# Performance work log

Hardware: AMD Instinct MI355X
Metric: run time of the kernel (lower is better)

The kernel has to match this reference:

```python
import jax, jax.numpy as jnp
import numpy as np

OUT_FEATURES = 11008
IN_FEATURES = 4096
GROUP_SIZE = 32
NUM_GROUPS = OUT_FEATURES * IN_FEATURES // GROUP_SIZE        # 1,409,024
NUM_PACKED = NUM_GROUPS * (GROUP_SIZE // 8 * 3)              # 16,908,288 bytes


def block_dequantize_3bit(weight_q3, weight_norm):
    """Unpack 3-bit codes (8 values per 3 bytes) and dequantize to fp32."""
    p = weight_q3.reshape(-1, 3).astype(jnp.int32)  # [N/8, 3] bytes
    b0, b1, b2 = p[:, 0], p[:, 1], p[:, 2]
    q = jnp.stack([
        b0 & 7,
        (b0 >> 3) & 7,
        ((b0 >> 6) & 3) | ((b1 & 1) << 2),
        (b1 >> 1) & 7,
        (b1 >> 4) & 7,
        ((b1 >> 7) & 1) | ((b2 & 3) << 1),
        (b2 >> 2) & 7,
        (b2 >> 5) & 7,
    ], axis=-1)                                     # [N/8, 8] codes in 0..7
    q = q.reshape(NUM_GROUPS, GROUP_SIZE).astype(jnp.float32)
    norm = weight_norm.astype(jnp.float32)[:, None]  # [num_groups, 1]
    w = (q / 7.0) * 2.0 * norm - norm                # map [0,7] -> [-norm, norm]
    return w.reshape(OUT_FEATURES, IN_FEATURES)


def setup_inputs() -> dict:
    key = jax.random.key(0)
    k1, k2, k3, k4 = jax.random.split(key, 4)
    x = jax.random.normal(k1, (4, 128, IN_FEATURES), dtype=jnp.float32)
    weight_q3 = jax.random.randint(k2, (NUM_PACKED,), 0, 256, dtype=jnp.int32)
    weight_norm = (jax.random.uniform(k3, (NUM_GROUPS,), dtype=jnp.float32) * 0.1 + 0.01).astype(jnp.float16)
    bias = jax.random.normal(k4, (OUT_FEATURES,), dtype=jnp.float32) * 0.02
    return {"x": x, "weight_q3": weight_q3, "weight_norm": weight_norm, "bias": bias}


def reference(x, weight_q3, weight_norm, bias):
    w = block_dequantize_3bit(weight_q3, weight_norm)  # [out, in] fp32
    return jnp.einsum('bsd,od->bso', x, w) + bias
```

## Files before the change

### kernel.cpp

```cpp
#include <hip/hip_runtime.h>
#include <hip/hip_fp16.h>

#define M_TOTAL 512
#define N_TOTAL 11008
#define K_TOTAL 4096
#define BM 64
#define BN 64
#define BK 64
#define NT (K_TOTAL / BK)
#define LDK 72

typedef short bf16x8 __attribute__((ext_vector_type(8)));
typedef float f32x4 __attribute__((ext_vector_type(4)));

__device__ __forceinline__ unsigned int pack2_bf16(float f0, float f1) {
    unsigned int u0 = __builtin_bit_cast(unsigned int, f0) + 0x8000u;
    unsigned int u1 = __builtin_bit_cast(unsigned int, f1) + 0x8000u;
    return (u0 >> 16) | (u1 & 0xFFFF0000u);
}

__device__ __forceinline__ void async_ld16(void* lds, const void* g) {
    __builtin_amdgcn_global_load_lds(
        (const __attribute__((address_space(1))) unsigned int*)g,
        (__attribute__((address_space(3))) unsigned int*)lds, 16, 0, 0);
}

__global__ void detect_norm_dtype(const void* __restrict__ wn, int* __restrict__ mode_out) {
    const int i = threadIdx.x;
    const unsigned short* u16 = (const unsigned short*)wn;
    const float* f32p = (const float*)wn;
    const float vb = __builtin_bit_cast(float, (unsigned int)u16[i] << 16);
    const float vh = __half2float(__builtin_bit_cast(__half, u16[i]));
    const float vf = f32p[i];
    const unsigned long long mb = __ballot(vb > 0.005f && vb < 0.12f);
    const unsigned long long mh = __ballot(vh > 0.005f && vh < 0.12f);
    const unsigned long long mf = __ballot(vf > 0.005f && vf < 0.12f);
    if (i == 0)
        *mode_out = (mb == ~0ull) ? 2 : ((mh == ~0ull) ? 1 : 0);
    (void)mf;
}

__global__ void __launch_bounds__(256)
convert_x_kernel(const float* __restrict__ x, unsigned short* __restrict__ xb) {
    const int i = (blockIdx.x * 256 + threadIdx.x) * 4;
    const float4 v = *(const float4*)&x[i];
    *(uint2*)&xb[i] = make_uint2(pack2_bf16(v.x, v.y), pack2_bf16(v.z, v.w));
}

__global__ void __launch_bounds__(256, 5)
l3b_gemm_pipe(const unsigned short* __restrict__ xb, const int* __restrict__ wq,
              const void* __restrict__ wnorm, const float* __restrict__ bias,
              float* __restrict__ out, const int* __restrict__ mode_ptr)
{
    __shared__ unsigned short As[2][BM * 64];
    __shared__ unsigned short Bs[2][BN * 64];

    const int mode = *mode_ptr;
    const int tid  = threadIdx.x;

    const int bid = blockIdx.x;
    const int w   = (bid & 7) * 172 + (bid >> 3);
    const int m0  = (w & 7) * BM;
    const int n0  = (w >> 3) * BN;

    const int wid  = tid >> 6;
    const int lane = tid & 63;
    const int quad = lane >> 4;
    const int lm   = lane & 15;
    const int wm   = (wid >> 1) * 32;
    const int wn   = (wid & 1) * 32;

    const int arow0 = wid * 8 + (lane >> 3);
    const int acol  = ((lane & 7) ^ ((lane >> 3) & 7)) * 8;
    const int aslot = (lane & 7) * 8;

    const int gin      = tid >> 1;
    const int half     = tid & 1;
    const int bn_local = gin >> 1;
    const int bkg      = gin & 1;
    const int c0       = bkg * 4 + half * 2;
    const int swz      = bn_local & 7;

    auto stageA = [&](int it, int buf) {
#pragma unroll
        for (int j = 0; j < 2; ++j) {
            const int row = arow0 + j * 32;
            async_ld16(&As[buf][(row << 6) + aslot],
                       &xb[(size_t)(m0 + row) * K_TOTAL + it * 64 + acol]);
        }
    };

    int2 w0a, w1a, w2a; float na;
    int2 w0b, w1b, w2b; float nb;

    auto loadNorm = [&](int g) -> float {
        if (mode == 0)      return ((const float*)wnorm)[g];
        else if (mode == 1) return __half2float(((const __half*)wnorm)[g]);
        else                return __builtin_bit_cast(float,
                               (unsigned int)((const unsigned short*)wnorm)[g] << 16);
    };
    auto loadB = [&](int it, int2& w0, int2& w1, int2& w2, float& nrm) {
        const int g    = (n0 + bn_local) * (K_TOTAL / 32) + it * 2 + bkg;
        const int base = g * 12 + half * 6;
        w0 = *(const int2*)&wq[base];
        w1 = *(const int2*)&wq[base + 2];
        w2 = *(const int2*)&wq[base + 4];
        nrm = loadNorm(g);
    };
    auto decodeB = [&](int2 w0, int2 w1, int2 w2, float nrm, int buf) {
        const float a = nrm * (2.0f / 7.0f);
        const float b = -nrm;
        const unsigned int bits0 =
            (unsigned)w0.x | ((unsigned)w0.y << 8) | ((unsigned)w1.x << 16);
        const unsigned int bits1 =
            (unsigned)w1.y | ((unsigned)w2.x << 8) | ((unsigned)w2.y << 16);
        unsigned int packs[8];
#pragma unroll
        for (int t3 = 0; t3 < 2; ++t3) {
            const unsigned int bits = t3 ? bits1 : bits0;
#pragma unroll
            for (int j = 0; j < 4; ++j) {
                const float f0 = fmaf((float)((bits >> (6 * j)) & 7), a, b);
                const float f1 = fmaf((float)((bits >> (6 * j + 3)) & 7), a, b);
                packs[t3 * 4 + j] = pack2_bf16(f0, f1);
            }
        }
        *(uint4*)&Bs[buf][(bn_local << 6) + ((c0 ^ swz) << 3)] =
            make_uint4(packs[0], packs[1], packs[2], packs[3]);
        *(uint4*)&Bs[buf][(bn_local << 6) + (((c0 + 1) ^ swz) << 3)] =
            make_uint4(packs[4], packs[5], packs[6], packs[7]);
    };

    f32x4 acc[2][2];
#pragma unroll
    for (int i = 0; i < 2; ++i)
#pragma unroll
        for (int j = 0; j < 2; ++j) acc[i][j] = (f32x4){0.f, 0.f, 0.f, 0.f};

    auto mfmaTile = [&](const unsigned short* Asb, const unsigned short* Bsb) {
#pragma unroll
        for (int ks = 0; ks < 2; ++ks) {
            const int cswz = (((ks * 4 + quad) ^ (lm & 7)) << 3);
            bf16x8 aF[2], bF[2];
#pragma unroll
            for (int mi = 0; mi < 2; ++mi)
                aF[mi] = *(const bf16x8*)&Asb[((wm + mi * 16 + lm) << 6) + cswz];
#pragma unroll
            for (int ni = 0; ni < 2; ++ni)
                bF[ni] = *(const bf16x8*)&Bsb[((wn + ni * 16 + lm) << 6) + cswz];
#pragma unroll
            for (int mi = 0; mi < 2; ++mi)
#pragma unroll
                for (int ni = 0; ni < 2; ++ni)
                    acc[mi][ni] = __builtin_amdgcn_mfma_f32_16x16x32_bf16(
                        aF[mi], bF[ni], acc[mi][ni], 0, 0, 0);
        }
    };

    stageA(0, 0);
    loadB(0, w0a, w1a, w2a, na);
    decodeB(w0a, w1a, w2a, na, 0);
    loadB(1, w0b, w1b, w2b, nb);
    __syncthreads();

    for (int it = 0; it < NT; it += 2) {
        if (it + 1 < NT) stageA(it + 1, 1);
        if (it + 2 < NT) loadB(it + 2, w0a, w1a, w2a, na);
        if (it + 1 < NT) decodeB(w0b, w1b, w2b, nb, 1);
        mfmaTile(As[0], Bs[0]);
        __syncthreads();

        if (it + 2 < NT) stageA(it + 2, 0);
        if (it + 3 < NT) loadB(it + 3, w0b, w1b, w2b, nb);
        if (it + 2 < NT) decodeB(w0a, w1a, w2a, na, 0);
        mfmaTile(As[1], Bs[1]);
        __syncthreads();
    }

#pragma unroll
    for (int ni = 0; ni < 2; ++ni) {
        const int o  = n0 + wn + ni * 16 + lm;
        const float bv = bias[o];
#pragma unroll
        for (int mi = 0; mi < 2; ++mi) {
#pragma unroll
            for (int r = 0; r < 4; ++r) {
                const int m = m0 + wm + mi * 16 + quad * 4 + r;
                out[m * N_TOTAL + o] = acc[mi][ni][r] + bv;
            }
        }
    }
}

__global__ void __launch_bounds__(256)
l3b_gemm_kernel(const float* __restrict__ x, const int* __restrict__ wq,
                const void* __restrict__ wnorm, const float* __restrict__ bias,
                float* __restrict__ out, const int* __restrict__ mode_ptr)
{
    __shared__ unsigned short As[128 * LDK];
    __shared__ unsigned short Bs[64 * LDK];

    const int mode = *mode_ptr;
    const int tid  = threadIdx.x;
    const int m0   = blockIdx.y * 128;
    const int n0   = blockIdx.x * 64;
    const int wid  = tid >> 6;
    const int lane = tid & 63;
    const int quad = lane >> 4;
    const int lm   = lane & 15;
    const int wm   = (wid >> 1) * 64;
    const int wn   = (wid & 1) * 32;

    f32x4 acc[4][2];
#pragma unroll
    for (int i = 0; i < 4; ++i)
#pragma unroll
        for (int j = 0; j < 2; ++j) acc[i][j] = (f32x4){0.f, 0.f, 0.f, 0.f};

    const int ar = tid >> 4;
    const int ac = (tid & 15) * 4;
    const int gin      = tid >> 1;
    const int half     = tid & 1;
    const int bn_local = gin >> 1;
    const int bkg      = gin & 1;

    for (int it = 0; it < NT; ++it) {
        const int k0 = it * BK;
        __syncthreads();
#pragma unroll
        for (int p = 0; p < 8; ++p) {
            const int row = p * 16 + ar;
            const float4 v = *(const float4*)&x[(m0 + row) * K_TOTAL + k0 + ac];
            *(uint2*)&As[row * LDK + ac] =
                make_uint2(pack2_bf16(v.x, v.y), pack2_bf16(v.z, v.w));
        }
        {
            const int g    = (n0 + bn_local) * (K_TOTAL / 32) + it * 2 + bkg;
            const int base = g * 12 + half * 6;
            const int2 w0 = *(const int2*)&wq[base];
            const int2 w1 = *(const int2*)&wq[base + 2];
            const int2 w2 = *(const int2*)&wq[base + 4];
            float nrm;
            if (mode == 0)      nrm = ((const float*)wnorm)[g];
            else if (mode == 1) nrm = __half2float(((const __half*)wnorm)[g]);
            else                nrm = __builtin_bit_cast(float,
                                    (unsigned int)((const unsigned short*)wnorm)[g] << 16);
            const float a = nrm * (2.0f / 7.0f);
            const float b = -nrm;
            const unsigned int bits0 =
                (unsigned)w0.x | ((unsigned)w0.y << 8) | ((unsigned)w1.x << 16);
            const unsigned int bits1 =
                (unsigned)w1.y | ((unsigned)w2.x << 8) | ((unsigned)w2.y << 16);
            unsigned int packs[8];
#pragma unroll
            for (int t3 = 0; t3 < 2; ++t3) {
                const unsigned int bits = t3 ? bits1 : bits0;
#pragma unroll
                for (int j = 0; j < 4; ++j) {
                    const float f0 = fmaf((float)((bits >> (6 * j)) & 7), a, b);
                    const float f1 = fmaf((float)((bits >> (6 * j + 3)) & 7), a, b);
                    packs[t3 * 4 + j] = pack2_bf16(f0, f1);
                }
            }
            unsigned int* dst = (unsigned int*)&Bs[bn_local * LDK + bkg * 32 + half * 16];
            *(uint4*)dst       = make_uint4(packs[0], packs[1], packs[2], packs[3]);
            *(uint4*)(dst + 4) = make_uint4(packs[4], packs[5], packs[6], packs[7]);
        }
        __syncthreads();
#pragma unroll
        for (int ks = 0; ks < 2; ++ks) {
            const int kb = ks * 32 + quad * 8;
            bf16x8 aF[4], bF[2];
#pragma unroll
            for (int mi = 0; mi < 4; ++mi)
                aF[mi] = *(const bf16x8*)&As[(wm + mi * 16 + lm) * LDK + kb];
#pragma unroll
            for (int ni = 0; ni < 2; ++ni)
                bF[ni] = *(const bf16x8*)&Bs[(wn + ni * 16 + lm) * LDK + kb];
#pragma unroll
            for (int mi = 0; mi < 4; ++mi)
#pragma unroll
                for (int ni = 0; ni < 2; ++ni)
                    acc[mi][ni] = __builtin_amdgcn_mfma_f32_16x16x32_bf16(
                        aF[mi], bF[ni], acc[mi][ni], 0, 0, 0);
        }
    }
#pragma unroll
    for (int ni = 0; ni < 2; ++ni) {
        const int o  = n0 + wn + ni * 16 + lm;
        const float bv = bias[o];
#pragma unroll
        for (int mi = 0; mi < 4; ++mi)
#pragma unroll
            for (int r = 0; r < 4; ++r) {
                const int m = m0 + wm + mi * 16 + quad * 4 + r;
                out[m * N_TOTAL + o] = acc[mi][ni][r] + bv;
            }
    }
}

extern "C" void kernel_launch(void* const* d_in, const int* in_sizes, int n_in,
                              void* d_out, int out_size, void* d_ws, size_t ws_size,
                              hipStream_t stream) {
    const float* x    = (const float*)d_in[0];
    const int*   wq   = (const int*)d_in[1];
    const void*  wn   = d_in[2];
    const float* bias = (const float*)d_in[3];
    float* out = (float*)d_out;
    int* mode = (int*)d_ws;

    detect_norm_dtype<<<1, 64, 0, stream>>>(wn, mode);

    const size_t need = 256 + (size_t)M_TOTAL * K_TOTAL * 2;
    if (ws_size >= need) {
        unsigned short* xb = (unsigned short*)((char*)d_ws + 256);
        convert_x_kernel<<<(M_TOTAL * K_TOTAL / 4) / 256, 256, 0, stream>>>(x, xb);
        l3b_gemm_pipe<<<(M_TOTAL / BM) * (N_TOTAL / BN), 256, 0, stream>>>(
            xb, wq, wn, bias, out, mode);
    } else {
        dim3 grid(N_TOTAL / 64, M_TOTAL / 128);
        l3b_gemm_kernel<<<grid, 256, 0, stream>>>(x, wq, wn, bias, out, mode);
    }
}
```

Measured before the change: 242.9 us.

## Use 128x64 tiles with 512 threads and fold dtype detection into GEMM

Doubles the M tile to 128 and the block to 512 threads, so each block covers twice the rows and each decoded weight tile is reused across more activations. B decode is split four ways per group, with each thread handling 8 codes instead of 16. The separate dtype-detection launch is replaced by each wave detecting the mode inline, which removes one kernel launch and a dependent global read. The trade-off is more LDS and registers per block and a grid that is half as large.

```diff
diff --git a/kernel.cpp b/kernel.cpp
--- a/kernel.cpp
+++ b/kernel.cpp
@@ -4,7 +4,7 @@
 #define M_TOTAL 512
 #define N_TOTAL 11008
 #define K_TOTAL 4096
-#define BM 64
+#define BM 128
 #define BN 64
 #define BK 64
 #define NT (K_TOTAL / BK)
@@ -25,19 +25,17 @@
         (__attribute__((address_space(3))) unsigned int*)lds, 16, 0, 0);
 }
 
-__global__ void detect_norm_dtype(const void* __restrict__ wn, int* __restrict__ mode_out) {
-    const int i = threadIdx.x;
+__device__ __forceinline__ int detect_mode_wave(const void* __restrict__ wn) {
+    const int lane = threadIdx.x & 63;
     const unsigned short* u16 = (const unsigned short*)wn;
     const float* f32p = (const float*)wn;
-    const float vb = __builtin_bit_cast(float, (unsigned int)u16[i] << 16);
-    const float vh = __half2float(__builtin_bit_cast(__half, u16[i]));
-    const float vf = f32p[i];
+    const float vb = __builtin_bit_cast(float, (unsigned int)u16[lane] << 16);
+    const float vh = __half2float(__builtin_bit_cast(__half, u16[lane]));
+    const float vf = f32p[lane];
     const unsigned long long mb = __ballot(vb > 0.005f && vb < 0.12f);
     const unsigned long long mh = __ballot(vh > 0.005f && vh < 0.12f);
-    const unsigned long long mf = __ballot(vf > 0.005f && vf < 0.12f);
-    if (i == 0)
-        *mode_out = (mb == ~0ull) ? 2 : ((mh == ~0ull) ? 1 : 0);
-    (void)mf;
+    (void)vf;
+    return (mb == ~0ull) ? 2 : ((mh == ~0ull) ? 1 : 0);
 }
 
 __global__ void __launch_bounds__(256)
@@ -47,51 +45,47 @@
     *(uint2*)&xb[i] = make_uint2(pack2_bf16(v.x, v.y), pack2_bf16(v.z, v.w));
 }
 
-__global__ void __launch_bounds__(256, 5)
+__global__ void __launch_bounds__(512, 6)
 l3b_gemm_pipe(const unsigned short* __restrict__ xb, const int* __restrict__ wq,
               const void* __restrict__ wnorm, const float* __restrict__ bias,
-              float* __restrict__ out, const int* __restrict__ mode_ptr)
+              float* __restrict__ out)
 {
     __shared__ unsigned short As[2][BM * 64];
     __shared__ unsigned short Bs[2][BN * 64];
 
-    const int mode = *mode_ptr;
     const int tid  = threadIdx.x;
+    const int mode = detect_mode_wave(wnorm);
 
     const int bid = blockIdx.x;
-    const int w   = (bid & 7) * 172 + (bid >> 3);
-    const int m0  = (w & 7) * BM;
-    const int n0  = (w >> 3) * BN;
+    const int w   = (bid & 7) * 86 + (bid >> 3);
+    const int m0  = (w & 3) * BM;
+    const int n0  = (w >> 2) * BN;
 
     const int wid  = tid >> 6;
     const int lane = tid & 63;
     const int quad = lane >> 4;
     const int lm   = lane & 15;
     const int wm   = (wid >> 1) * 32;
-    const int wn   = (wid & 1) * 32;
+    const int wn_  = (wid & 1) * 32;
 
     const int arow0 = wid * 8 + (lane >> 3);
     const int acol  = ((lane & 7) ^ ((lane >> 3) & 7)) * 8;
     const int aslot = (lane & 7) * 8;
 
-    const int gin      = tid >> 1;
-    const int half     = tid & 1;
-    const int bn_local = gin >> 1;
-    const int bkg      = gin & 1;
-    const int c0       = bkg * 4 + half * 2;
-    const int swz      = bn_local & 7;
+    const int gl   = tid >> 2;
+    const int sub  = tid & 3;
+    const int bn_l = gl >> 1;
+    const int kg   = gl & 1;
+    const int ldsB = (bn_l << 6) + ((((kg * 4 + sub)) ^ (bn_l & 7)) << 3);
 
     auto stageA = [&](int it, int buf) {
 #pragma unroll
         for (int j = 0; j < 2; ++j) {
-            const int row = arow0 + j * 32;
+            const int row = arow0 + j * 64;
             async_ld16(&As[buf][(row << 6) + aslot],
                        &xb[(size_t)(m0 + row) * K_TOTAL + it * 64 + acol]);
         }
     };
-
-    int2 w0a, w1a, w2a; float na;
-    int2 w0b, w1b, w2b; float nb;
 
     auto loadNorm = [&](int g) -> float {
         if (mode == 0)      return ((const float*)wnorm)[g];
@@ -99,36 +93,25 @@
         else                return __builtin_bit_cast(float,
                                (unsigned int)((const unsigned short*)wnorm)[g] << 16);
     };
-    auto loadB = [&](int it, int2& w0, int2& w1, int2& w2, float& nrm) {
-        const int g    = (n0 + bn_local) * (K_TOTAL / 32) + it * 2 + bkg;
-        const int base = g * 12 + half * 6;
-        w0 = *(const int2*)&wq[base];
-        w1 = *(const int2*)&wq[base + 2];
-        w2 = *(const int2*)&wq[base + 4];
+    auto loadB = [&](int it, int& b0, int& b1, int& b2, float& nrm) {
+        const int g    = (n0 + bn_l) * (K_TOTAL / 32) + it * 2 + kg;
+        const int base = g * 12 + sub * 3;
+        b0 = wq[base]; b1 = wq[base + 1]; b2 = wq[base + 2];
         nrm = loadNorm(g);
     };
-    auto decodeB = [&](int2 w0, int2 w1, int2 w2, float nrm, int buf) {
+    auto decodeB = [&](int b0, int b1, int b2, float nrm, int buf) {
         const float a = nrm * (2.0f / 7.0f);
         const float b = -nrm;
-        const unsigned int bits0 =
-            (unsigned)w0.x | ((unsigned)w0.y << 8) | ((unsigned)w1.x << 16);
-        const unsigned int bits1 =
-            (unsigned)w1.y | ((unsigned)w2.x << 8) | ((unsigned)w2.y << 16);
-        unsigned int packs[8];
-#pragma unroll
-        for (int t3 = 0; t3 < 2; ++t3) {
-            const unsigned int bits = t3 ? bits1 : bits0;
-#pragma unroll
-            for (int j = 0; j < 4; ++j) {
-                const float f0 = fmaf((float)((bits >> (6 * j)) & 7), a, b);
-                const float f1 = fmaf((float)((bits >> (6 * j + 3)) & 7), a, b);
-                packs[t3 * 4 + j] = pack2_bf16(f0, f1);
-            }
-        }
-        *(uint4*)&Bs[buf][(bn_local << 6) + ((c0 ^ swz) << 3)] =
-            make_uint4(packs[0], packs[1], packs[2], packs[3]);
-        *(uint4*)&Bs[buf][(bn_local << 6) + (((c0 + 1) ^ swz) << 3)] =
-            make_uint4(packs[4], packs[5], packs[6], packs[7]);
+        const unsigned int bits =
+            (unsigned)b0 | ((unsigned)b1 << 8) | ((unsigned)b2 << 16);
+        unsigned int packs[4];
+#pragma unroll
+        for (int j = 0; j < 4; ++j) {
+            const float f0 = fmaf((float)((bits >> (6 * j)) & 7), a, b);
+            const float f1 = fmaf((float)((bits >> (6 * j + 3)) & 7), a, b);
+            packs[j] = pack2_bf16(f0, f1);
+        }
+        *(uint4*)&Bs[buf][ldsB] = make_uint4(packs[0], packs[1], packs[2], packs[3]);
     };
 
     f32x4 acc[2][2];
@@ -147,7 +130,7 @@
                 aF[mi] = *(const bf16x8*)&Asb[((wm + mi * 16 + lm) << 6) + cswz];
 #pragma unroll
             for (int ni = 0; ni < 2; ++ni)
-                bF[ni] = *(const bf16x8*)&Bsb[((wn + ni * 16 + lm) << 6) + cswz];
+                bF[ni] = *(const bf16x8*)&Bsb[((wn_ + ni * 16 + lm) << 6) + cswz];
 #pragma unroll
             for (int mi = 0; mi < 2; ++mi)
 #pragma unroll
@@ -157,29 +140,32 @@
         }
     };
 
+    int b0a, b1a, b2a; float na;
+    int b0b, b1b, b2b; float nb;
+
     stageA(0, 0);
-    loadB(0, w0a, w1a, w2a, na);
-    decodeB(w0a, w1a, w2a, na, 0);
-    loadB(1, w0b, w1b, w2b, nb);
+    loadB(0, b0a, b1a, b2a, na);
+    decodeB(b0a, b1a, b2a, na, 0);
+    loadB(1, b0b, b1b, b2b, nb);
     __syncthreads();
 
     for (int it = 0; it < NT; it += 2) {
         if (it + 1 < NT) stageA(it + 1, 1);
-        if (it + 2 < NT) loadB(it + 2, w0a, w1a, w2a, na);
-        if (it + 1 < NT) decodeB(w0b, w1b, w2b, nb, 1);
+        if (it + 2 < NT) loadB(it + 2, b0a, b1a, b2a, na);
+        if (it + 1 < NT) decodeB(b0b, b1b, b2b, nb, 1);
         mfmaTile(As[0], Bs[0]);
         __syncthreads();
 
         if (it + 2 < NT) stageA(it + 2, 0);
-        if (it + 3 < NT) loadB(it + 3, w0b, w1b, w2b, nb);
-        if (it + 2 < NT) decodeB(w0a, w1a, w2a, na, 0);
+        if (it + 3 < NT) loadB(it + 3, b0b, b1b, b2b, nb);
+        if (it + 2 < NT) decodeB(b0a, b1a, b2a, na, 0);
         mfmaTile(As[1], Bs[1]);
         __syncthreads();
     }
 
 #pragma unroll
     for (int ni = 0; ni < 2; ++ni) {
-        const int o  = n0 + wn + ni * 16 + lm;
+        const int o  = n0 + wn_ + ni * 16 + lm;
         const float bv = bias[o];
 #pragma unroll
         for (int mi = 0; mi < 2; ++mi) {
@@ -195,12 +181,12 @@
 __global__ void __launch_bounds__(256)
 l3b_gemm_kernel(const float* __restrict__ x, const int* __restrict__ wq,
                 const void* __restrict__ wnorm, const float* __restrict__ bias,
-                float* __restrict__ out, const int* __restrict__ mode_ptr)
+                float* __restrict__ out)
 {
     __shared__ unsigned short As[128 * LDK];
     __shared__ unsigned short Bs[64 * LDK];
 
-    const int mode = *mode_ptr;
+    const int mode = detect_mode_wave(wnorm);
     const int tid  = threadIdx.x;
     const int m0   = blockIdx.y * 128;
     const int n0   = blockIdx.x * 64;
@@ -307,18 +293,15 @@
     const void*  wn   = d_in[2];
     const float* bias = (const float*)d_in[3];
     float* out = (float*)d_out;
-    int* mode = (int*)d_ws;
-
-    detect_norm_dtype<<<1, 64, 0, stream>>>(wn, mode);
 
     const size_t need = 256 + (size_t)M_TOTAL * K_TOTAL * 2;
     if (ws_size >= need) {
         unsigned short* xb = (unsigned short*)((char*)d_ws + 256);
         convert_x_kernel<<<(M_TOTAL * K_TOTAL / 4) / 256, 256, 0, stream>>>(x, xb);
-        l3b_gemm_pipe<<<(M_TOTAL / BM) * (N_TOTAL / BN), 256, 0, stream>>>(
-            xb, wq, wn, bias, out, mode);
+        l3b_gemm_pipe<<<(M_TOTAL / BM) * (N_TOTAL / BN), 512, 0, stream>>>(
+            xb, wq, wn, bias, out);
     } else {
         dim3 grid(N_TOTAL / 64, M_TOTAL / 128);
-        l3b_gemm_kernel<<<grid, 256, 0, stream>>>(x, wq, wn, bias, out, mode);
-    }
-}
+        l3b_gemm_kernel<<<grid, 256, 0, stream>>>(x, wq, wn, bias, out);
+    }
+}
```

New measurement: 198.3 us. -18.3%, faster.
